# Optimization experiments

Measured on AMD Instinct MI355X. Metric: run time of the kernel, lower is better.

The kernel has to match this reference:

```python
import jax, jax.numpy as jnp
import numpy as np

B, S, D, H, HD = 2, 2048, 2048, 16, 128  # batch, seq, embed, heads, head_dim


def setup_inputs() -> dict:
    key = jax.random.key(0)
    k0, k1, k2 = jax.random.split(key, 3)
    hidden_states = jax.random.normal(k0, (B, S, D), dtype=jnp.float32)
    # fused QKV projection: [D, H*HD + 2*HD] (multi-query: single shared K and V head)
    W_attn = jax.random.normal(k1, (D, H * HD + 2 * HD), dtype=jnp.float32) * 0.02
    b_attn = jnp.zeros((H * HD + 2 * HD,), dtype=jnp.float32)
    W_proj = jax.random.normal(k2, (D, D), dtype=jnp.float32) * 0.02
    b_proj = jnp.zeros((D,), dtype=jnp.float32)
    # causal mask, broadcastable to (B, Q, H, K); True = attend
    attention_mask = jnp.tril(jnp.ones((S, S), dtype=bool))[None, :, None, :]
    return {
        "hidden_states": hidden_states,
        "W_attn": W_attn,
        "b_attn": b_attn,
        "W_proj": W_proj,
        "b_proj": b_proj,
        "attention_mask": attention_mask,
    }


def reference(hidden_states, W_attn, b_attn, W_proj, b_proj, attention_mask):
    # fused QKV, then split into Q (H heads) and shared K/V (multi-query)
    qkv = hidden_states @ W_attn + b_attn          # (B, S, H*HD + 2*HD)
    q = qkv[..., : H * HD].reshape(B, S, H, HD)    # (B, Q, H, hd)
    key_t = qkv[..., H * HD : H * HD + HD]         # (B, K, hd) shared K head
    value = qkv[..., H * HD + HD :]                # (B, K, hd) shared V head

    # dtype == softmax_dtype (fp32) -> upcast=False, unscale=1
    scale_factor = 1.0 / (HD ** 0.5)               # scale_attn_weights
    attn_weights = jnp.einsum("bqhd,bkd->bqhk", q, key_t) * scale_factor
    mask_value = jnp.finfo(jnp.float32).min
    attn_weights = jnp.where(attention_mask, attn_weights, mask_value)
    attn_weights = jax.nn.softmax(attn_weights, axis=-1)

    attn_output = jnp.einsum("bqhk,bkd->bqhd", attn_weights, value)
    attn_output = attn_output.reshape(B, S, H * HD)
    return attn_output @ W_proj + b_proj           # (B, S, D)
```

## Files before the change

kernel.cpp:

```cpp
#include <hip/hip_runtime.h>
#include <math.h>

constexpr int cB  = 2;
constexpr int cS  = 2048;
constexpr int cD  = 2048;
constexpr int cH  = 16;
constexpr int cHD = 128;
constexpr int cNQKV = cH * cHD + 2 * cHD;

typedef __attribute__((ext_vector_type(8))) short bf16x8;
typedef __attribute__((ext_vector_type(4))) float f32x4;

__device__ __forceinline__ short f2bf(float f) {
    union { float f; unsigned u; } v; v.f = f;
    unsigned r = (v.u + 0x7FFFu + ((v.u >> 16) & 1u)) >> 16;
    return (short)r;
}

typedef __attribute__((address_space(3))) void lds_t;
typedef const __attribute__((address_space(1))) void gbl_t;
__device__ __forceinline__ void gld16(const void* g, void* l) {
    __builtin_amdgcn_global_load_lds((gbl_t*)g, (lds_t*)l, 16, 0, 0);
}

__global__ __launch_bounds__(256) void conv_bf16(
    const float* __restrict__ src, short* __restrict__ dst)
{
    size_t i = ((size_t)blockIdx.x * 256 + threadIdx.x) * 8;
    float4 a = *(const float4*)(src + i);
    float4 b = *(const float4*)(src + i + 4);
    bf16x8 o;
    o[0] = f2bf(a.x); o[1] = f2bf(a.y); o[2] = f2bf(a.z); o[3] = f2bf(a.w);
    o[4] = f2bf(b.x); o[5] = f2bf(b.y); o[6] = f2bf(b.z); o[7] = f2bf(b.w);
    *(bf16x8*)(dst + i) = o;
}

__global__ __launch_bounds__(256) void transpose_bf16(
    const float* __restrict__ src, short* __restrict__ dst, int K, int N)
{
    __shared__ short t[32][33];
    const int n0 = blockIdx.x * 32, k0 = blockIdx.y * 32;
    const int x = threadIdx.x & 31, y = threadIdx.x >> 5;
#pragma unroll
    for (int i = 0; i < 4; ++i)
        t[y + 8 * i][x] = f2bf(src[(size_t)(k0 + y + 8 * i) * N + n0 + x]);
    __syncthreads();
#pragma unroll
    for (int i = 0; i < 4; ++i)
        dst[(size_t)(n0 + y + 8 * i) * K + k0 + x] = t[x][y + 8 * i];
}

template<bool BF16_OUT>
__global__ __launch_bounds__(256) void gemm_mfma(
    const short* __restrict__ A, const short* __restrict__ Bt,
    const float* __restrict__ bias, void* __restrict__ Cout,
    int M, int N, int K, float qscale, int qcols)
{
    __shared__ short As[128 * 32];
    __shared__ short Bs[128 * 32];

    const int tid = threadIdx.x;
    const int lane = tid & 63, n16 = lane & 15, quad = lane >> 4;
    const int wave = tid >> 6, wm = wave >> 1, wn = wave & 1;
    const int m0 = blockIdx.y * 128, n0 = blockIdx.x * 128;

    f32x4 acc[4][4];
#pragma unroll
    for (int i = 0; i < 4; ++i)
#pragma unroll
        for (int j = 0; j < 4; ++j) acc[i][j] = 0.0f;

    const int s0 = tid, s1 = tid + 256;
    const short* Ag0 = A  + (size_t)(m0 + (s0 >> 2)) * K + (s0 & 3) * 8;
    const short* Ag1 = A  + (size_t)(m0 + (s1 >> 2)) * K + (s1 & 3) * 8;
    const short* Bg0 = Bt + (size_t)(n0 + (s0 >> 2)) * K + (s0 & 3) * 8;
    const short* Bg1 = Bt + (size_t)(n0 + (s1 >> 2)) * K + (s1 & 3) * 8;

    for (int k0 = 0; k0 < K; k0 += 32) {
        gld16(Ag0 + k0, &As[s0 * 8]);
        gld16(Ag1 + k0, &As[s1 * 8]);
        gld16(Bg0 + k0, &Bs[s0 * 8]);
        gld16(Bg1 + k0, &Bs[s1 * 8]);
        __syncthreads();
        bf16x8 af[4], bfr[4];
#pragma unroll
        for (int mt = 0; mt < 4; ++mt)
            af[mt] = *(const bf16x8*)&As[(wm * 64 + mt * 16 + n16) * 32 + quad * 8];
#pragma unroll
        for (int nt = 0; nt < 4; ++nt)
            bfr[nt] = *(const bf16x8*)&Bs[(wn * 64 + nt * 16 + n16) * 32 + quad * 8];
#pragma unroll
        for (int mt = 0; mt < 4; ++mt)
#pragma unroll
            for (int nt = 0; nt < 4; ++nt)
                acc[mt][nt] = __builtin_amdgcn_mfma_f32_16x16x32_bf16(
                    af[mt], bfr[nt], acc[mt][nt], 0, 0, 0);
        __syncthreads();
    }

#pragma unroll
    for (int nt = 0; nt < 4; ++nt) {
        const int col = n0 + wn * 64 + nt * 16 + n16;
        const float bv = bias[col];
        const float sc = (col < qcols) ? qscale : 1.0f;
#pragma unroll
        for (int mt = 0; mt < 4; ++mt)
#pragma unroll
            for (int r = 0; r < 4; ++r) {
                const int row = m0 + wm * 64 + mt * 16 + quad * 4 + r;
                const float v = (acc[mt][nt][r] + bv) * sc;
                if (BF16_OUT) ((short*)Cout)[(size_t)row * N + col] = f2bf(v);
                else          ((float*)Cout)[(size_t)row * N + col] = v;
            }
    }
}

__global__ __launch_bounds__(256) void prep_v(
    const short* __restrict__ qkvb, short* __restrict__ Vt)
{
    const int b  = blockIdx.y;
    const int k0 = blockIdx.x * 64;
    const int t  = threadIdx.x;
#pragma unroll
    for (int i = 0; i < 32; ++i) {
        int idx = i * 256 + t;
        int hd = idx >> 6, key = idx & 63;
        Vt[((size_t)b * cHD + hd) * cS + k0 + key] =
            qkvb[((size_t)(b * cS + k0 + key)) * cNQKV + cH * cHD + cHD + hd];
    }
}

__global__ __launch_bounds__(256) void attn_mfma(
    const short* __restrict__ qkvb, const short* __restrict__ Vt,
    short* __restrict__ out)
{
    const int tid  = threadIdx.x;
    const int wave = tid >> 6;
    const int lane = tid & 63;
    const int n16  = lane & 15;
    const int quad = lane >> 4;
    const int qt = (int)gridDim.x - 1 - (int)blockIdx.x;
    const int h  = blockIdx.y;
    const int b  = blockIdx.z;
    const int q0 = qt * 64 + wave * 16;

    __shared__ __align__(16) short Ks[8192];
    __shared__ __align__(16) short Vs[8192];
    __shared__ __align__(16) short Ps[4][16][72];

    const int part = lane & 3;
    const int krow = lane >> 2;

    bf16x8 qf[4];
    {
        const short* qbase = qkvb + ((size_t)(b * cS) + q0 + n16) * cNQKV + h * cHD + quad * 8;
#pragma unroll
        for (int ch = 0; ch < 4; ++ch) qf[ch] = *(const bf16x8*)(qbase + ch * 32);
    }

    f32x4 oc[8];
#pragma unroll
    for (int on = 0; on < 8; ++on) oc[on] = 0.0f;
    float lp[4] = {0.0f, 0.0f, 0.0f, 0.0f};

    const short* kglob = qkvb + (size_t)b * cS * cNQKV + cH * cHD;
    const short* vbase = Vt + (size_t)b * cHD * cS;
    const int nkt = qt + 1;

    for (int kt = 0; kt < nkt; ++kt) {
        const int k0 = kt * 64;

        __syncthreads();
        {
            const short* kr = kglob + (size_t)(k0 + wave * 16 + krow) * cNQKV + part * 8;
#pragma unroll
            for (int j = 0; j < 4; ++j)
                gld16(kr + j * 32, &Ks[(j * 4 + wave) * 512]);
        }
        {
#pragma unroll
            for (int j = 0; j < 4; ++j) {
                const int idx = j * 4 + wave;
                const int c2 = idx >> 3;
                const int hd = (idx & 7) * 16 + krow;
                gld16(vbase + (size_t)hd * cS + k0 + c2 * 32 + part * 8,
                      &Vs[idx * 512]);
            }
        }
        __syncthreads();

        f32x4 sc[4];
#pragma unroll
        for (int nt = 0; nt < 4; ++nt) sc[nt] = 0.0f;
#pragma unroll
        for (int nt = 0; nt < 4; ++nt) {
#pragma unroll
            for (int ch = 0; ch < 4; ++ch) {
                bf16x8 kf = *(const bf16x8*)&Ks[(ch * 64 + nt * 16 + n16) * 32 + quad * 8];
                sc[nt] = __builtin_amdgcn_mfma_f32_16x16x32_bf16(qf[ch], kf, sc[nt], 0, 0, 0);
            }
        }

        if (kt == nkt - 1) {
#pragma unroll
            for (int nt = 0; nt < 4; ++nt)
#pragma unroll
                for (int r = 0; r < 4; ++r) {
                    int row = q0 + quad * 4 + r;
                    int col = k0 + nt * 16 + n16;
                    if (col > row) sc[nt][r] = -1e30f;
                }
        }

#pragma unroll
        for (int r = 0; r < 4; ++r)
#pragma unroll
            for (int nt = 0; nt < 4; ++nt) {
                float p = __expf(sc[nt][r]);
                lp[r] += p;
                Ps[wave][quad * 4 + r][nt * 16 + n16] = f2bf(p);
            }

        bf16x8 pf0 = *(const bf16x8*)&Ps[wave][n16][quad * 8];
        bf16x8 pf1 = *(const bf16x8*)&Ps[wave][n16][32 + quad * 8];

#pragma unroll
        for (int on = 0; on < 8; ++on) {
            bf16x8 vf0 = *(const bf16x8*)&Vs[(on * 16 + n16) * 32 + quad * 8];
            bf16x8 vf1 = *(const bf16x8*)&Vs[(128 * 32) + (on * 16 + n16) * 32 + quad * 8];
            oc[on] = __builtin_amdgcn_mfma_f32_16x16x32_bf16(pf0, vf0, oc[on], 0, 0, 0);
            oc[on] = __builtin_amdgcn_mfma_f32_16x16x32_bf16(pf1, vf1, oc[on], 0, 0, 0);
        }
    }

    float inv[4];
#pragma unroll
    for (int r = 0; r < 4; ++r) {
        float t = lp[r];
        t += __shfl_xor(t, 1);
        t += __shfl_xor(t, 2);
        t += __shfl_xor(t, 4);
        t += __shfl_xor(t, 8);
        inv[r] = 1.0f / t;
    }
    short* obase = out + ((size_t)(b * cS) + q0) * cD + h * cHD;
#pragma unroll
    for (int on = 0; on < 8; ++on)
#pragma unroll
        for (int r = 0; r < 4; ++r)
            obase[(size_t)(quad * 4 + r) * cD + on * 16 + n16] = f2bf(oc[on][r] * inv[r]);
}

extern "C" void kernel_launch(void* const* d_in, const int* in_sizes, int n_in,
                              void* d_out, int out_size, void* d_ws, size_t ws_size,
                              hipStream_t stream)
{
    const float* hidden = (const float*)d_in[0];
    const float* W_attn = (const float*)d_in[1];
    const float* b_attn = (const float*)d_in[2];
    const float* W_proj = (const float*)d_in[3];
    const float* b_proj = (const float*)d_in[4];
    float* out = (float*)d_out;

    const int M = cB * cS;
    short* qkvb = (short*)d_ws;
    short* Ah   = qkvb + (size_t)M * cNQKV;
    short* Wb   = Ah   + (size_t)M * cD;
    short* Wpb  = Wb   + (size_t)cNQKV * cD;
    short* Vt   = Wpb  + (size_t)cD * cD;
    short* attno = Ah;

    const float scale = 0.088388347648318447f;

    conv_bf16<<<(size_t)M * cD / 2048, 256, 0, stream>>>(hidden, Ah);
    transpose_bf16<<<dim3(cNQKV / 32, cD / 32), 256, 0, stream>>>(W_attn, Wb, cD, cNQKV);
    transpose_bf16<<<dim3(cD / 32, cD / 32), 256, 0, stream>>>(W_proj, Wpb, cD, cD);

    gemm_mfma<true><<<dim3(cNQKV / 128, M / 128), 256, 0, stream>>>(
        Ah, Wb, b_attn, qkvb, M, cNQKV, cD, scale, cH * cHD);

    prep_v<<<dim3(cS / 64, cB), 256, 0, stream>>>(qkvb, Vt);

    attn_mfma<<<dim3(cS / 64, cH, cB), 256, 0, stream>>>(qkvb, Vt, attno);

    gemm_mfma<false><<<dim3(cD / 128, M / 128), 256, 0, stream>>>(
        attno, Wpb, b_proj, out, M, cD, cD, 1.0f, 0);
}
```

Before: 368.7 us.

## Split causal KV range across waves with per-wave LDS tiles and cross-wave reduction

The attention kernel now has each of the four waves own all 64 query rows and take an interleaved subset of 32-key tiles. Each wave loads its own K and V tiles into private, XOR-swizzled LDS regions, so the block-wide barriers inside the key loop go away. Partial outputs and row sums are combined through LDS at the end. This removes per-iteration syncs and reuses each K/V fragment across four query subtiles, at the cost of much higher register pressure (128 accumulator floats plus 16 Q fragments per lane), 64KB of LDS, and an extra reduction pass.

```diff
diff --git a/kernel.cpp b/kernel.cpp
--- a/kernel.cpp
+++ b/kernel.cpp
@@ -134,6 +134,8 @@
     const short* __restrict__ qkvb, const short* __restrict__ Vt,
     short* __restrict__ out)
 {
+    __shared__ short lds16[32768];
+
     const int tid  = threadIdx.x;
     const int wave = tid >> 6;
     const int lane = tid & 63;
@@ -142,113 +144,170 @@
     const int qt = (int)gridDim.x - 1 - (int)blockIdx.x;
     const int h  = blockIdx.y;
     const int b  = blockIdx.z;
-    const int q0 = qt * 64 + wave * 16;
-
-    __shared__ __align__(16) short Ks[8192];
-    __shared__ __align__(16) short Vs[8192];
-    __shared__ __align__(16) short Ps[4][16][72];
-
-    const int part = lane & 3;
-    const int krow = lane >> 2;
-
-    bf16x8 qf[4];
+    const int q0b = qt * 64;
+
+    short* Kbuf = &lds16[wave * 8192];
+    short* Vbuf = &lds16[wave * 8192 + 4096];
+    short* Ps   = Kbuf;
+
+    bf16x8 qf[4][4];
     {
-        const short* qbase = qkvb + ((size_t)(b * cS) + q0 + n16) * cNQKV + h * cHD + quad * 8;
-#pragma unroll
-        for (int ch = 0; ch < 4; ++ch) qf[ch] = *(const bf16x8*)(qbase + ch * 32);
-    }
-
-    f32x4 oc[8];
-#pragma unroll
-    for (int on = 0; on < 8; ++on) oc[on] = 0.0f;
-    float lp[4] = {0.0f, 0.0f, 0.0f, 0.0f};
+        const short* qb = qkvb + ((size_t)(b * cS) + q0b + n16) * cNQKV + h * cHD + quad * 8;
+#pragma unroll
+        for (int mt = 0; mt < 4; ++mt)
+#pragma unroll
+            for (int ch = 0; ch < 4; ++ch)
+                qf[mt][ch] = *(const bf16x8*)(qb + (size_t)(mt * 16) * cNQKV + ch * 32);
+    }
+
+    f32x4 oc[4][8];
+#pragma unroll
+    for (int mt = 0; mt < 4; ++mt)
+#pragma unroll
+        for (int on = 0; on < 8; ++on) oc[mt][on] = 0.0f;
+    float lp[4][4] = {};
 
     const short* kglob = qkvb + (size_t)b * cS * cNQKV + cH * cHD;
     const short* vbase = Vt + (size_t)b * cHD * cS;
-    const int nkt = qt + 1;
-
-    for (int kt = 0; kt < nkt; ++kt) {
-        const int k0 = kt * 64;
-
+    const int nkt = 2 * (qt + 1);
+
+    const int kkey_lo = lane >> 4;
+    const int ksw     = lane & 15;
+    const int vhd_lo  = lane >> 2;
+    const int vsw     = lane & 3;
+
+    for (int t = wave; t < nkt; t += 4) {
+        const int k0 = t * 32;
+
+#pragma unroll
+        for (int j = 0; j < 8; ++j) {
+            const int key = j * 4 + kkey_lo;
+            const int c16 = ksw ^ (key & 15);
+            gld16(kglob + (size_t)(k0 + key) * cNQKV + c16 * 8, &Kbuf[j * 512 + lane * 8]);
+        }
+#pragma unroll
+        for (int j = 0; j < 8; ++j) {
+            const int hd = j * 16 + vhd_lo;
+            const int kc = vsw ^ ((hd >> 2) & 3);
+            gld16(vbase + (size_t)hd * cS + k0 + kc * 8, &Vbuf[j * 512 + lane * 8]);
+        }
+        __asm volatile("s_waitcnt vmcnt(0)" ::: "memory");
+
+        f32x4 sc[4][2];
+#pragma unroll
+        for (int mt = 0; mt < 4; ++mt) { sc[mt][0] = 0.0f; sc[mt][1] = 0.0f; }
+#pragma unroll
+        for (int nt = 0; nt < 2; ++nt) {
+            const int key = nt * 16 + n16;
+#pragma unroll
+            for (int ch = 0; ch < 4; ++ch) {
+                bf16x8 kf = *(const bf16x8*)&Kbuf[(key * 16 + (((ch * 4 + quad)) ^ n16)) * 8];
+#pragma unroll
+                for (int mt = 0; mt < 4; ++mt)
+                    sc[mt][nt] = __builtin_amdgcn_mfma_f32_16x16x32_bf16(
+                        qf[mt][ch], kf, sc[mt][nt], 0, 0, 0);
+            }
+        }
+
+        if (k0 + 31 > q0b) {
+#pragma unroll
+            for (int mt = 0; mt < 4; ++mt)
+#pragma unroll
+                for (int nt = 0; nt < 2; ++nt)
+#pragma unroll
+                    for (int r = 0; r < 4; ++r) {
+                        int row = q0b + mt * 16 + quad * 4 + r;
+                        int col = k0 + nt * 16 + n16;
+                        if (col > row) sc[mt][nt][r] = -1e30f;
+                    }
+        }
+
+#pragma unroll
+        for (int mt = 0; mt < 4; ++mt)
+#pragma unroll
+            for (int r = 0; r < 4; ++r)
+#pragma unroll
+                for (int nt = 0; nt < 2; ++nt) {
+                    float p = __expf(sc[mt][nt][r]);
+                    lp[mt][r] += p;
+                    Ps[(mt * 16 + quad * 4 + r) * 40 + nt * 16 + n16] = f2bf(p);
+                }
+
+        bf16x8 pf[4];
+#pragma unroll
+        for (int mt = 0; mt < 4; ++mt)
+            pf[mt] = *(const bf16x8*)&Ps[(mt * 16 + n16) * 40 + quad * 8];
+
+#pragma unroll
+        for (int on = 0; on < 8; ++on) {
+            const int hd = on * 16 + n16;
+            bf16x8 vf = *(const bf16x8*)&Vbuf[(hd * 4 + (quad ^ (n16 >> 2))) * 8];
+#pragma unroll
+            for (int mt = 0; mt < 4; ++mt)
+                oc[mt][on] = __builtin_amdgcn_mfma_f32_16x16x32_bf16(
+                    pf[mt], vf, oc[mt][on], 0, 0, 0);
+        }
+    }
+
+    __syncthreads();
+
+    float* Lf = (float*)&lds16[4096];
+    {
+#pragma unroll
+        for (int mt = 0; mt < 4; ++mt)
+#pragma unroll
+            for (int r = 0; r < 4; ++r) {
+                float s = lp[mt][r];
+                s += __shfl_xor(s, 1);
+                s += __shfl_xor(s, 2);
+                s += __shfl_xor(s, 4);
+                s += __shfl_xor(s, 8);
+                lp[mt][r] = s;
+            }
+        if (n16 == 0) {
+#pragma unroll
+            for (int mt = 0; mt < 4; ++mt)
+#pragma unroll
+                for (int r = 0; r < 4; ++r)
+                    Lf[wave * 64 + mt * 16 + quad * 4 + r] = lp[mt][r];
+        }
+    }
+
+    float inv[4];
+    short* obase = out + ((size_t)(b * cS) + q0b + wave * 16) * cD + h * cHD;
+
+#pragma unroll
+    for (int pass = 0; pass < 4; ++pass) {
         __syncthreads();
-        {
-            const short* kr = kglob + (size_t)(k0 + wave * 16 + krow) * cNQKV + part * 8;
-#pragma unroll
-            for (int j = 0; j < 4; ++j)
-                gld16(kr + j * 32, &Ks[(j * 4 + wave) * 512]);
-        }
-        {
-#pragma unroll
-            for (int j = 0; j < 4; ++j) {
-                const int idx = j * 4 + wave;
-                const int c2 = idx >> 3;
-                const int hd = (idx & 7) * 16 + krow;
-                gld16(vbase + (size_t)hd * cS + k0 + c2 * 32 + part * 8,
-                      &Vs[idx * 512]);
+#pragma unroll
+        for (int mt = 0; mt < 4; ++mt)
+#pragma unroll
+            for (int oi = 0; oi < 2; ++oi)
+                *(f32x4*)&lds16[wave * 8192 + (mt * 2 + oi) * 512 + lane * 8] =
+                    oc[mt][2 * pass + oi];
+        __syncthreads();
+        if (pass == 0) {
+#pragma unroll
+            for (int r = 0; r < 4; ++r) {
+                float lt = 0.0f;
+#pragma unroll
+                for (int wv = 0; wv < 4; ++wv)
+                    lt += Lf[wv * 64 + wave * 16 + quad * 4 + r];
+                inv[r] = 1.0f / lt;
             }
         }
-        __syncthreads();
-
-        f32x4 sc[4];
-#pragma unroll
-        for (int nt = 0; nt < 4; ++nt) sc[nt] = 0.0f;
-#pragma unroll
-        for (int nt = 0; nt < 4; ++nt) {
-#pragma unroll
-            for (int ch = 0; ch < 4; ++ch) {
-                bf16x8 kf = *(const bf16x8*)&Ks[(ch * 64 + nt * 16 + n16) * 32 + quad * 8];
-                sc[nt] = __builtin_amdgcn_mfma_f32_16x16x32_bf16(qf[ch], kf, sc[nt], 0, 0, 0);
-            }
-        }
-
-        if (kt == nkt - 1) {
-#pragma unroll
-            for (int nt = 0; nt < 4; ++nt)
-#pragma unroll
-                for (int r = 0; r < 4; ++r) {
-                    int row = q0 + quad * 4 + r;
-                    int col = k0 + nt * 16 + n16;
-                    if (col > row) sc[nt][r] = -1e30f;
-                }
-        }
-
-#pragma unroll
-        for (int r = 0; r < 4; ++r)
-#pragma unroll
-            for (int nt = 0; nt < 4; ++nt) {
-                float p = __expf(sc[nt][r]);
-                lp[r] += p;
-                Ps[wave][quad * 4 + r][nt * 16 + n16] = f2bf(p);
-            }
-
-        bf16x8 pf0 = *(const bf16x8*)&Ps[wave][n16][quad * 8];
-        bf16x8 pf1 = *(const bf16x8*)&Ps[wave][n16][32 + quad * 8];
-
-#pragma unroll
-        for (int on = 0; on < 8; ++on) {
-            bf16x8 vf0 = *(const bf16x8*)&Vs[(on * 16 + n16) * 32 + quad * 8];
-            bf16x8 vf1 = *(const bf16x8*)&Vs[(128 * 32) + (on * 16 + n16) * 32 + quad * 8];
-            oc[on] = __builtin_amdgcn_mfma_f32_16x16x32_bf16(pf0, vf0, oc[on], 0, 0, 0);
-            oc[on] = __builtin_amdgcn_mfma_f32_16x16x32_bf16(pf1, vf1, oc[on], 0, 0, 0);
-        }
-    }
-
-    float inv[4];
-#pragma unroll
-    for (int r = 0; r < 4; ++r) {
-        float t = lp[r];
-        t += __shfl_xor(t, 1);
-        t += __shfl_xor(t, 2);
-        t += __shfl_xor(t, 4);
-        t += __shfl_xor(t, 8);
-        inv[r] = 1.0f / t;
-    }
-    short* obase = out + ((size_t)(b * cS) + q0) * cD + h * cHD;
-#pragma unroll
-    for (int on = 0; on < 8; ++on)
-#pragma unroll
-        for (int r = 0; r < 4; ++r)
-            obase[(size_t)(quad * 4 + r) * cD + on * 16 + n16] = f2bf(oc[on][r] * inv[r]);
+#pragma unroll
+        for (int oi = 0; oi < 2; ++oi) {
+            f32x4 s = 0.0f;
+#pragma unroll
+            for (int wv = 0; wv < 4; ++wv)
+                s += *(const f32x4*)&lds16[wv * 8192 + (wave * 2 + oi) * 512 + lane * 8];
+            const int col = (2 * pass + oi) * 16 + n16;
+#pragma unroll
+            for (int r = 0; r < 4; ++r)
+                obase[(size_t)(quad * 4 + r) * cD + col] = f2bf(s[r] * inv[r]);
+        }
+    }
 }
 
 extern "C" void kernel_launch(void* const* d_in, const int* in_sizes, int n_in,
```

New measurement: 399.9 us. 1.08x slower.
